# Optimization experiments

Hardware: AMD Instinct MI355X
Metric: run time of the kernel (lower is better)

## Reference

```python
import jax, jax.numpy as jnp
import numpy as np

N_NODES = 50000
N_EDGES = 500000
IN_DIM = 128
H1, C1 = 4, 64   # layer1: heads=4, out=64, concat -> 256
H2, C2 = 1, 64   # layer2: heads=1, out=64


def setup_inputs() -> dict:
    key = jax.random.key(0)
    ks = jax.random.split(key, 16)
    p = lambda k, shp: (jax.random.normal(k, shp, dtype=jnp.float32) * 0.1)
    return {
        "x": jax.random.normal(ks[0], (N_NODES, IN_DIM), dtype=jnp.float32),
        "edge_index": jax.random.randint(ks[1], (2, N_EDGES), 0, N_NODES, dtype=jnp.int32),
        "edge_attr": jax.random.uniform(ks[2], (N_EDGES, 1), dtype=jnp.float32),
        # layer 1 params
        "W1": p(ks[3], (IN_DIM, H1 * C1)),
        "We1": p(ks[4], (1, H1 * C1)),
        "as1": p(ks[5], (H1, C1)),
        "ad1": p(ks[6], (H1, C1)),
        "ae1": p(ks[7], (H1, C1)),
        "b1": jnp.zeros((H1 * C1,), dtype=jnp.float32),
        # layer 2 params
        "W2": p(ks[8], (H1 * C1, H2 * C2)),
        "We2": p(ks[9], (1, H2 * C2)),
        "as2": p(ks[10], (H2, C2)),
        "ad2": p(ks[11], (H2, C2)),
        "ae2": p(ks[12], (H2, C2)),
        "b2": jnp.zeros((H2 * C2,), dtype=jnp.float32),
    }


def _add_self_loops(src, dst, edge_attr, n):
    # PyG fill_value='mean': loop edge_attr = mean of incoming edge attrs per node
    cnt = jax.ops.segment_sum(jnp.ones((src.shape[0],), edge_attr.dtype), dst, num_segments=n)
    loop_attr = jax.ops.segment_sum(edge_attr, dst, num_segments=n) / jnp.maximum(cnt, 1.0)[:, None]
    idx = jnp.arange(n, dtype=src.dtype)
    return (jnp.concatenate([src, idx]), jnp.concatenate([dst, idx]),
            jnp.concatenate([edge_attr, loop_attr], axis=0))


def _gat_conv(x, src, dst, edge_attr, W, We, a_src, a_dst, a_edge, bias, heads, out_ch):
    n = x.shape[0]
    h = (x @ W).reshape(n, heads, out_ch)                      # [N,H,C]
    e = (edge_attr @ We).reshape(-1, heads, out_ch)            # [E,H,C]
    alpha = ((h * a_src).sum(-1)[src]                          # gather src score
             + (h * a_dst).sum(-1)[dst]                        # gather dst score
             + (e * a_edge).sum(-1))                           # [E,H]
    alpha = jax.nn.leaky_relu(alpha, 0.2)
    m = jax.ops.segment_max(alpha, dst, num_segments=n)        # per-target max
    alpha = jnp.exp(alpha - m[dst])
    denom = jax.ops.segment_sum(alpha, dst, num_segments=n)
    alpha = alpha / (denom[dst] + 1e-16)
    out = jax.ops.segment_sum(h[src] * alpha[..., None], dst, num_segments=n)
    return out.reshape(n, heads * out_ch) + bias


def reference(x, edge_index, edge_attr, W1, We1, as1, ad1, ae1, b1,
              W2, We2, as2, ad2, ae2, b2):
    src, dst = edge_index[0], edge_index[1]
    src, dst, ea = _add_self_loops(src, dst, edge_attr, x.shape[0])
    h = jax.nn.elu(_gat_conv(x, src, dst, ea, W1, We1, as1, ad1, ae1, b1, H1, C1))
    return _gat_conv(h, src, dst, ea, W2, We2, as2, ad2, ae2, b2, H2, C2)
```

## Files before the change

### kernel.cpp

```cpp
#include <hip/hip_runtime.h>
#include <math.h>

#define NN 50000
#define NE 500000
#define DIM 128
#define HC1 256
#define HC2 64
#define BCAP 64

typedef __attribute__((ext_vector_type(8))) short short8;
typedef __attribute__((ext_vector_type(4))) float floatx4;


__device__ __forceinline__ unsigned short f2bf(float f) {
  unsigned int u = __float_as_uint(f);
  unsigned int r = (u + 0x7FFFu + ((u >> 16) & 1u)) >> 16;
  return (unsigned short)r;
}
__device__ __forceinline__ float bf2f(unsigned short s) {
  return __uint_as_float(((unsigned int)s) << 16);
}


__global__ void k_bucket(const int* __restrict__ src, const int* __restrict__ dst,
                         const float* __restrict__ ea,
                         unsigned long long* __restrict__ P,
                         int2* __restrict__ ebuf) {
  int e = blockIdx.x * blockDim.x + threadIdx.x;
  if (e < NE) {
    int d = dst[e];
    float eav = ea[e];
    unsigned long long fx = (unsigned long long)(unsigned int)__float2uint_rn(eav * 16777216.0f);
    unsigned long long old = atomicAdd(&P[d], (1ULL << 40) | fx);
    int pos = (int)(old >> 40);
    if (pos < BCAP)
      ebuf[d * BCAP + pos] = make_int2(src[e], __float_as_int(eav));
  }
}

__device__ __forceinline__ void decodeP(unsigned long long p, int& cn, float& lea) {
  int c = (int)(p >> 40);
  cn = (c < BCAP) ? c : BCAP;
  float asum = (float)(p & 0xFFFFFFFFFFULL) * (1.0f / 16777216.0f);
  lea = asum / fmaxf((float)c, 1.0f);
}


__device__ __forceinline__ float waveReduce(float v) {
  v += __shfl_down(v, 32);
  v += __shfl_down(v, 16);
  v += __shfl_down(v, 8);
  v += __shfl_down(v, 4);
  v += __shfl_down(v, 2);
  v += __shfl_down(v, 1);
  return v;
}


__global__ __launch_bounds__(256) void k_prep(const float* __restrict__ W1,
                                              const float* __restrict__ W2,
                                              const float* __restrict__ We1,
                                              const float* __restrict__ ae1,
                                              const float* __restrict__ We2,
                                              const float* __restrict__ ae2,
                                              unsigned short* __restrict__ W1T,
                                              unsigned short* __restrict__ W2T,
                                              float* __restrict__ ce) {
  int b = blockIdx.x, t = threadIdx.x;
  if (b < 128) {
    int idx = b * 256 + t;
    int n = idx >> 7, k = idx & 127;
    W1T[idx] = f2bf(W1[k * 256 + n]);
  } else if (b < 192) {
    int idx = (b - 128) * 256 + t;
    int n = idx >> 8, k = idx & 255;
    W2T[idx] = f2bf(W2[k * 64 + n]);
  } else {
    int h = t >> 6, lane = t & 63;
    float p = We1[h * 64 + lane] * ae1[h * 64 + lane];
    p = waveReduce(p);
    if (lane == 0) ce[h] = p;
    if (h == 0) {
      float q = We2[lane] * ae2[lane];
      q = waveReduce(q);
      if (lane == 0) ce[4] = q;
    }
  }
}


__global__ __launch_bounds__(256) void k_gemm1m(const float* __restrict__ x,
                                                const unsigned short* __restrict__ W1T,
                                                const float* __restrict__ as1,
                                                const float* __restrict__ ad1,
                                                unsigned short* __restrict__ h1b,
                                                float* __restrict__ ss1,
                                                float* __restrict__ sd1) {
  __shared__ unsigned short As[64 * 136];
  int t = threadIdx.x;
  int wave = t >> 6, lane = t & 63;
  int q = lane >> 4, ln = lane & 15;
  int m0 = blockIdx.x * 64;
  int n0 = wave * 64;

  short8 bfr[4][4];
#pragma unroll
  for (int c = 0; c < 4; c++)
#pragma unroll
    for (int ks = 0; ks < 4; ks++)
      bfr[c][ks] = *(const short8*)&W1T[(n0 + c * 16 + ln) * 128 + ks * 32 + q * 8];

#pragma unroll
  for (int rep = 0; rep < 8; rep++) {
    int chunk = t + 256 * rep;
    int m = chunk >> 5, kk = (chunk & 31) * 4;
    int gr = m0 + m;
    float4 v = (gr < NN) ? *(const float4*)&x[gr * DIM + kk]
                         : make_float4(0.f, 0.f, 0.f, 0.f);
    ushort4 o;
    o.x = f2bf(v.x); o.y = f2bf(v.y); o.z = f2bf(v.z); o.w = f2bf(v.w);
    *(ushort4*)&As[m * 136 + kk] = o;
  }
  __syncthreads();

  floatx4 acc[4][4];
#pragma unroll
  for (int r = 0; r < 4; r++)
#pragma unroll
    for (int c = 0; c < 4; c++) acc[r][c] = (floatx4){0.f, 0.f, 0.f, 0.f};

#pragma unroll
  for (int ks = 0; ks < 4; ks++) {
    short8 afr[4];
#pragma unroll
    for (int r = 0; r < 4; r++)
      afr[r] = *(const short8*)&As[(r * 16 + ln) * 136 + ks * 32 + q * 8];
#pragma unroll
    for (int r = 0; r < 4; r++)
#pragma unroll
      for (int c = 0; c < 4; c++)
        acc[r][c] = __builtin_amdgcn_mfma_f32_16x16x32_bf16(afr[r], bfr[c][ks], acc[r][c], 0, 0, 0);
  }

  float as1v[4], ad1v[4];
#pragma unroll
  for (int c = 0; c < 4; c++) {
    as1v[c] = as1[n0 + c * 16 + ln];
    ad1v[c] = ad1[n0 + c * 16 + ln];
  }

#pragma unroll
  for (int r = 0; r < 4; r++) {
#pragma unroll
    for (int i = 0; i < 4; i++) {
      int gm = m0 + r * 16 + q * 4 + i;
      if (gm < NN) {
#pragma unroll
        for (int c = 0; c < 4; c++)
          h1b[gm * HC1 + n0 + c * 16 + ln] = f2bf(acc[r][c][i]);
      }
      float ps = acc[r][0][i] * as1v[0];
      float pd = acc[r][0][i] * ad1v[0];
#pragma unroll
      for (int c = 1; c < 4; c++) {
        ps = fmaf(acc[r][c][i], as1v[c], ps);
        pd = fmaf(acc[r][c][i], ad1v[c], pd);
      }
#pragma unroll
      for (int m = 1; m < 16; m <<= 1) {
        ps += __shfl_xor(ps, m);
        pd += __shfl_xor(pd, m);
      }
      if (ln == 0 && gm < NN) {
        ss1[gm * 4 + wave] = ps;
        sd1[gm * 4 + wave] = pd;
      }
    }
  }
}

__global__ __launch_bounds__(256) void k_gemm2m(const unsigned short* __restrict__ out1b,
                                                const unsigned short* __restrict__ W2T,
                                                const float* __restrict__ as2,
                                                const float* __restrict__ ad2,
                                                unsigned short* __restrict__ h2b,
                                                float* __restrict__ ss2,
                                                float* __restrict__ sd2) {
  __shared__ unsigned short As[64 * 264];
  __shared__ float ssp[4][64], sdp[4][64];
  int t = threadIdx.x;
  int wave = t >> 6, lane = t & 63;
  int q = lane >> 4, ln = lane & 15;
  int m0 = blockIdx.x * 64;
  int n0 = wave * 16;

  short8 bfr[8];
#pragma unroll
  for (int ks = 0; ks < 8; ks++)
    bfr[ks] = *(const short8*)&W2T[(n0 + ln) * 256 + ks * 32 + q * 8];

  short8 zero8 = {0, 0, 0, 0, 0, 0, 0, 0};
#pragma unroll
  for (int rep = 0; rep < 8; rep++) {
    int chunk = t + 256 * rep;
    int m = chunk >> 5, kk = (chunk & 31) * 8;
    int gr = m0 + m;
    short8 vv = (gr < NN) ? *(const short8*)&out1b[gr * 256 + kk] : zero8;
    *(short8*)&As[m * 264 + kk] = vv;
  }
  __syncthreads();

  floatx4 acc[4];
#pragma unroll
  for (int r = 0; r < 4; r++) acc[r] = (floatx4){0.f, 0.f, 0.f, 0.f};

#pragma unroll
  for (int ks = 0; ks < 8; ks++) {
#pragma unroll
    for (int r = 0; r < 4; r++) {
      short8 afr = *(const short8*)&As[(r * 16 + ln) * 264 + ks * 32 + q * 8];
      acc[r] = __builtin_amdgcn_mfma_f32_16x16x32_bf16(afr, bfr[ks], acc[r], 0, 0, 0);
    }
  }

  float as2v = as2[n0 + ln], ad2v = ad2[n0 + ln];
#pragma unroll
  for (int r = 0; r < 4; r++) {
#pragma unroll
    for (int i = 0; i < 4; i++) {
      int gm = m0 + r * 16 + q * 4 + i;
      if (gm < NN) h2b[gm * HC2 + n0 + ln] = f2bf(acc[r][i]);
      float ps = acc[r][i] * as2v;
      float pd = acc[r][i] * ad2v;
#pragma unroll
      for (int m = 1; m < 16; m <<= 1) {
        ps += __shfl_xor(ps, m);
        pd += __shfl_xor(pd, m);
      }
      if (ln == 0) {
        ssp[wave][r * 16 + q * 4 + i] = ps;
        sdp[wave][r * 16 + q * 4 + i] = pd;
      }
    }
  }
  __syncthreads();
  if (t < 64) {
    int gm = m0 + t;
    if (gm < NN) {
      ss2[gm] = ssp[0][t] + ssp[1][t] + ssp[2][t] + ssp[3][t];
      sd2[gm] = sdp[0][t] + sdp[1][t] + sdp[2][t] + sdp[3][t];
    }
  }
}


__global__ __launch_bounds__(256) void k_agg1(const unsigned short* __restrict__ h1b,
                                              const unsigned long long* __restrict__ P,
                                              const int2* __restrict__ ebuf,
                                              const float* __restrict__ ss1,
                                              const float* __restrict__ sd1,
                                              const float* __restrict__ ce,
                                              const float* __restrict__ b1,
                                              unsigned short* __restrict__ out1b) {
  int v = (blockIdx.x * blockDim.x + threadIdx.x) >> 6;
  int lane = threadIdx.x & 63;
  int h = lane >> 4;
  int c4 = lane * 4;
  int l16 = lane & 15;
  int vu = __builtin_amdgcn_readfirstlane(v);
  int cn; float lea;
  decodeP(P[vu], cn, lea);
  cn = __builtin_amdgcn_readfirstlane(cn);
  int beg = vu * BCAP;
  int end = beg + cn;
  float sdh = sd1[vu * 4 + h];
  float ceh = ce[h];
  float4 acc = make_float4(0.f, 0.f, 0.f, 0.f);
  float l = 0.f;

  for (int base = beg; base < end; base += 16) {
    int2 meta = ebuf[base + l16];
#pragma unroll
    for (int b4 = 0; b4 < 4; b4++) {
      if (base + b4 * 4 >= end) break;
      float ssv[4], ea4[4];
      ushort4 u[4];
      bool vld[4];
#pragma unroll
      for (int jj = 0; jj < 4; jj++) {
        int j = b4 * 4 + jj;
        bool val = (base + j < end);
        int sj = val ? __builtin_amdgcn_readlane(meta.x, j) : 0;
        ea4[jj] = __int_as_float(__builtin_amdgcn_readlane(meta.y, j));
        vld[jj] = val;
        ssv[jj] = ss1[sj * 4 + h];
        u[jj] = *(const ushort4*)&h1b[sj * HC1 + c4];
      }
#pragma unroll
      for (int jj = 0; jj < 4; jj++) {
        float x = fmaf(ea4[jj], ceh, ssv[jj] + sdh);
        x = fmaxf(x, 0.2f * x);
        float a = vld[jj] ? __expf(x) : 0.f;
        l += a;
        acc.x = fmaf(a, bf2f(u[jj].x), acc.x);
        acc.y = fmaf(a, bf2f(u[jj].y), acc.y);
        acc.z = fmaf(a, bf2f(u[jj].z), acc.z);
        acc.w = fmaf(a, bf2f(u[jj].w), acc.w);
      }
    }
  }
  {
    float x = fmaf(lea, ceh, ss1[vu * 4 + h] + sdh);
    x = fmaxf(x, 0.2f * x);
    float a = __expf(x);
    ushort4 u = *(const ushort4*)&h1b[vu * HC1 + c4];
    l += a;
    acc.x = fmaf(a, bf2f(u.x), acc.x);
    acc.y = fmaf(a, bf2f(u.y), acc.y);
    acc.z = fmaf(a, bf2f(u.z), acc.z);
    acc.w = fmaf(a, bf2f(u.w), acc.w);
  }
  float inv = 1.f / (l + 1e-16f);
  float4 bv = *(const float4*)&b1[c4];
  float4 o;
  o.x = acc.x * inv + bv.x;
  o.y = acc.y * inv + bv.y;
  o.z = acc.z * inv + bv.z;
  o.w = acc.w * inv + bv.w;
  o.x = (o.x > 0.f) ? o.x : expm1f(o.x);
  o.y = (o.y > 0.f) ? o.y : expm1f(o.y);
  o.z = (o.z > 0.f) ? o.z : expm1f(o.z);
  o.w = (o.w > 0.f) ? o.w : expm1f(o.w);
  ushort4 ob;
  ob.x = f2bf(o.x); ob.y = f2bf(o.y); ob.z = f2bf(o.z); ob.w = f2bf(o.w);
  *(ushort4*)&out1b[vu * HC1 + c4] = ob;
}

__global__ __launch_bounds__(256) void k_agg2(const unsigned short* __restrict__ h2b,
                                              const unsigned long long* __restrict__ P,
                                              const int2* __restrict__ ebuf,
                                              const float* __restrict__ ss2,
                                              const float* __restrict__ sd2,
                                              const float* __restrict__ ce,
                                              const float* __restrict__ b2,
                                              float* __restrict__ out) {
  int v = (blockIdx.x * blockDim.x + threadIdx.x) >> 6;
  int lane = threadIdx.x & 63;
  int g = lane >> 4;
  int c = lane & 15;
  int l16 = lane & 15;
  int vu = __builtin_amdgcn_readfirstlane(v);
  int cn; float lea;
  decodeP(P[vu], cn, lea);
  cn = __builtin_amdgcn_readfirstlane(cn);
  int beg = vu * BCAP;
  int end = beg + cn;
  float sdv = sd2[vu];
  float cev = ce[4];
  float4 acc = make_float4(0.f, 0.f, 0.f, 0.f);
  float l = 0.f;

  for (int base = beg; base < end; base += 16) {
    int nb = end - base;
    int2 meta = ebuf[base + l16];
    float ssv[4], eav[4];
    bool vld[4];
    ushort4 u[4];
#pragma unroll
    for (int sub = 0; sub < 4; sub++) {
      int j = sub * 4 + g;
      bool val = (j < nb);
      int sj = val ? __shfl(meta.x, j) : 0;
      eav[sub] = __int_as_float(__shfl(meta.y, j));
      vld[sub] = val;
      ssv[sub] = ss2[sj];
      u[sub] = *(const ushort4*)&h2b[sj * HC2 + c * 4];
    }
#pragma unroll
    for (int sub = 0; sub < 4; sub++) {
      float x = fmaf(eav[sub], cev, ssv[sub] + sdv);
      x = fmaxf(x, 0.2f * x);
      float a = vld[sub] ? __expf(x) : 0.f;
      l += a;
      acc.x = fmaf(a, bf2f(u[sub].x), acc.x);
      acc.y = fmaf(a, bf2f(u[sub].y), acc.y);
      acc.z = fmaf(a, bf2f(u[sub].z), acc.z);
      acc.w = fmaf(a, bf2f(u[sub].w), acc.w);
    }
  }
#pragma unroll
  for (int m = 16; m <= 32; m <<= 1) {
    acc.x += __shfl_xor(acc.x, m);
    acc.y += __shfl_xor(acc.y, m);
    acc.z += __shfl_xor(acc.z, m);
    acc.w += __shfl_xor(acc.w, m);
    l += __shfl_xor(l, m);
  }
  {
    float x = fmaf(lea, cev, ss2[vu] + sdv);
    x = fmaxf(x, 0.2f * x);
    float a = __expf(x);
    ushort4 us = *(const ushort4*)&h2b[vu * HC2 + c * 4];
    l += a;
    acc.x = fmaf(a, bf2f(us.x), acc.x);
    acc.y = fmaf(a, bf2f(us.y), acc.y);
    acc.z = fmaf(a, bf2f(us.z), acc.z);
    acc.w = fmaf(a, bf2f(us.w), acc.w);
  }
  if (g == 0) {
    float inv = 1.f / (l + 1e-16f);
    float4 bv = *(const float4*)&b2[c * 4];
    float4 o;
    o.x = acc.x * inv + bv.x;
    o.y = acc.y * inv + bv.y;
    o.z = acc.z * inv + bv.z;
    o.w = acc.w * inv + bv.w;
    *(float4*)&out[vu * HC2 + c * 4] = o;
  }
}


extern "C" void kernel_launch(void* const* d_in, const int* in_sizes, int n_in,
                              void* d_out, int out_size, void* d_ws, size_t ws_size,
                              hipStream_t stream) {
  const float* x   = (const float*)d_in[0];
  const int*   ei  = (const int*)d_in[1];
  const float* ea  = (const float*)d_in[2];
  const float* W1  = (const float*)d_in[3];
  const float* We1 = (const float*)d_in[4];
  const float* as1 = (const float*)d_in[5];
  const float* ad1 = (const float*)d_in[6];
  const float* ae1 = (const float*)d_in[7];
  const float* b1  = (const float*)d_in[8];
  const float* W2  = (const float*)d_in[9];
  const float* We2 = (const float*)d_in[10];
  const float* as2 = (const float*)d_in[11];
  const float* ad2 = (const float*)d_in[12];
  const float* ae2 = (const float*)d_in[13];
  const float* b2  = (const float*)d_in[14];
  const int* srcp = ei;
  const int* dstp = ei + NE;

  char* w = (char*)d_ws;
  unsigned long long* P = (unsigned long long*)(w + 0);
  float* ce      = (float*)(w + 400064);
  float* ss1     = (float*)(w + 400576);
  float* sd1     = (float*)(w + 1200576);
  float* ss2     = (float*)(w + 2000576);
  float* sd2     = (float*)(w + 2200576);
  int2*  ebuf    = (int2*) (w + 2400640);
  unsigned short* h1b   = (unsigned short*)(w + 28000640);
  unsigned short* out1b = (unsigned short*)(w + 53600640);
  unsigned short* h2b   = (unsigned short*)(w + 79200640);
  unsigned short* W1T   = (unsigned short*)(w + 85600640);
  unsigned short* W2T   = (unsigned short*)(w + 85666176);

  hipMemsetAsync(w, 0, 400000, stream);

  k_bucket<<<(NE + 255) / 256, 256, 0, stream>>>(srcp, dstp, ea, P, ebuf);
  k_prep<<<193, 256, 0, stream>>>(W1, W2, We1, ae1, We2, ae2, W1T, W2T, ce);

  k_gemm1m<<<(NN + 63) / 64, 256, 0, stream>>>(x, W1T, as1, ad1, h1b, ss1, sd1);
  k_agg1<<<(NN * 64 + 255) / 256, 256, 0, stream>>>(h1b, P, ebuf, ss1, sd1, ce, b1, out1b);

  k_gemm2m<<<(NN + 63) / 64, 256, 0, stream>>>(out1b, W2T, as2, ad2, h2b, ss2, sd2);
  k_agg2<<<(NN * 64 + 255) / 256, 256, 0, stream>>>(h2b, P, ebuf, ss2, sd2, ce, b2,
                                                    (float*)d_out);
}
```

Before: 232.7 us.

## Split layer-1 aggregation per head with head-major features and packed edge metadata

Stores layer-1 transformed features in a head-major layout and launches the first aggregation as one wave per (head, node), with blocks ordered head-first so each pass gathers from a smaller per-head feature slice. Packs each bucketed edge record into 32 bits (16-bit source index, 16-bit quantized edge attribute) to halve metadata traffic in both aggregations. Merges the edge bucketing kernel with the weight preparation kernel into one launch. The per-head split repeats metadata and score loads four times, and the quantized edge attribute adds small numerical error.

```diff
diff --git a/kernel.cpp b/kernel.cpp
--- a/kernel.cpp
+++ b/kernel.cpp
@@ -20,31 +20,6 @@
 __device__ __forceinline__ float bf2f(unsigned short s) {
   return __uint_as_float(((unsigned int)s) << 16);
 }
-
-
-__global__ void k_bucket(const int* __restrict__ src, const int* __restrict__ dst,
-                         const float* __restrict__ ea,
-                         unsigned long long* __restrict__ P,
-                         int2* __restrict__ ebuf) {
-  int e = blockIdx.x * blockDim.x + threadIdx.x;
-  if (e < NE) {
-    int d = dst[e];
-    float eav = ea[e];
-    unsigned long long fx = (unsigned long long)(unsigned int)__float2uint_rn(eav * 16777216.0f);
-    unsigned long long old = atomicAdd(&P[d], (1ULL << 40) | fx);
-    int pos = (int)(old >> 40);
-    if (pos < BCAP)
-      ebuf[d * BCAP + pos] = make_int2(src[e], __float_as_int(eav));
-  }
-}
-
-__device__ __forceinline__ void decodeP(unsigned long long p, int& cn, float& lea) {
-  int c = (int)(p >> 40);
-  cn = (c < BCAP) ? c : BCAP;
-  float asum = (float)(p & 0xFFFFFFFFFFULL) * (1.0f / 16777216.0f);
-  lea = asum / fmaxf((float)c, 1.0f);
-}
-
 
 __device__ __forceinline__ float waveReduce(float v) {
   v += __shfl_down(v, 32);
@@ -56,23 +31,50 @@
   return v;
 }
 
-
-__global__ __launch_bounds__(256) void k_prep(const float* __restrict__ W1,
-                                              const float* __restrict__ W2,
-                                              const float* __restrict__ We1,
-                                              const float* __restrict__ ae1,
-                                              const float* __restrict__ We2,
-                                              const float* __restrict__ ae2,
-                                              unsigned short* __restrict__ W1T,
-                                              unsigned short* __restrict__ W2T,
-                                              float* __restrict__ ce) {
+__device__ __forceinline__ void decodeP(unsigned long long p, int& cn, float& lea) {
+  int c = (int)(p >> 40);
+  cn = (c < BCAP) ? c : BCAP;
+  float asum = (float)(p & 0xFFFFFFFFFFULL) * (1.0f / 16777216.0f);
+  lea = asum / fmaxf((float)c, 1.0f);
+}
+
+
+#define NBUCKET ((NE + 255) / 256)
+
+__global__ __launch_bounds__(256) void k_build(const int* __restrict__ src,
+                                               const int* __restrict__ dst,
+                                               const float* __restrict__ ea,
+                                               unsigned long long* __restrict__ P,
+                                               unsigned int* __restrict__ ebuf,
+                                               const float* __restrict__ W1,
+                                               const float* __restrict__ W2,
+                                               const float* __restrict__ We1,
+                                               const float* __restrict__ ae1,
+                                               const float* __restrict__ We2,
+                                               const float* __restrict__ ae2,
+                                               unsigned short* __restrict__ W1T,
+                                               unsigned short* __restrict__ W2T,
+                                               float* __restrict__ ce) {
   int b = blockIdx.x, t = threadIdx.x;
-  if (b < 128) {
-    int idx = b * 256 + t;
+  if (b < NBUCKET) {
+    int e = b * 256 + t;
+    if (e < NE) {
+      int d = dst[e];
+      float eav = ea[e];
+      unsigned long long fx = (unsigned long long)(unsigned int)__float2uint_rn(eav * 16777216.0f);
+      unsigned long long old = atomicAdd(&P[d], (1ULL << 40) | fx);
+      int pos = (int)(old >> 40);
+      unsigned int ea16 = __float2uint_rn(eav * 65536.0f);
+      if (ea16 > 65535u) ea16 = 65535u;
+      if (pos < BCAP)
+        ebuf[d * BCAP + pos] = (ea16 << 16) | (unsigned int)src[e];
+    }
+  } else if (b < NBUCKET + 128) {
+    int idx = (b - NBUCKET) * 256 + t;
     int n = idx >> 7, k = idx & 127;
     W1T[idx] = f2bf(W1[k * 256 + n]);
-  } else if (b < 192) {
-    int idx = (b - 128) * 256 + t;
+  } else if (b < NBUCKET + 192) {
+    int idx = (b - NBUCKET - 128) * 256 + t;
     int n = idx >> 8, k = idx & 255;
     W2T[idx] = f2bf(W2[k * 64 + n]);
   } else {
@@ -93,7 +95,7 @@
                                                 const unsigned short* __restrict__ W1T,
                                                 const float* __restrict__ as1,
                                                 const float* __restrict__ ad1,
-                                                unsigned short* __restrict__ h1b,
+                                                unsigned short* __restrict__ h1h,
                                                 float* __restrict__ ss1,
                                                 float* __restrict__ sd1) {
   __shared__ unsigned short As[64 * 136];
@@ -157,7 +159,7 @@
       if (gm < NN) {
 #pragma unroll
         for (int c = 0; c < 4; c++)
-          h1b[gm * HC1 + n0 + c * 16 + ln] = f2bf(acc[r][c][i]);
+          h1h[(wave * NN + gm) * 64 + c * 16 + ln] = f2bf(acc[r][c][i]);
       }
       float ps = acc[r][0][i] * as1v[0];
       float pd = acc[r][0][i] * ad1v[0];
@@ -254,47 +256,45 @@
 }
 
 
-__global__ __launch_bounds__(256) void k_agg1(const unsigned short* __restrict__ h1b,
+__global__ __launch_bounds__(256) void k_agg1(const unsigned short* __restrict__ h1h,
                                               const unsigned long long* __restrict__ P,
-                                              const int2* __restrict__ ebuf,
+                                              const unsigned int* __restrict__ ebuf,
                                               const float* __restrict__ ss1,
                                               const float* __restrict__ sd1,
                                               const float* __restrict__ ce,
                                               const float* __restrict__ b1,
                                               unsigned short* __restrict__ out1b) {
-  int v = (blockIdx.x * blockDim.x + threadIdx.x) >> 6;
-  int lane = threadIdx.x & 63;
-  int h = lane >> 4;
-  int c4 = lane * 4;
+  int wave = threadIdx.x >> 6, lane = threadIdx.x & 63;
+  int head = blockIdx.x / 12500;
+  int vu = (blockIdx.x % 12500) * 4 + wave;
   int l16 = lane & 15;
-  int vu = __builtin_amdgcn_readfirstlane(v);
   int cn; float lea;
   decodeP(P[vu], cn, lea);
   cn = __builtin_amdgcn_readfirstlane(cn);
   int beg = vu * BCAP;
   int end = beg + cn;
-  float sdh = sd1[vu * 4 + h];
-  float ceh = ce[h];
-  float4 acc = make_float4(0.f, 0.f, 0.f, 0.f);
-  float l = 0.f;
+  float sdh = sd1[vu * 4 + head];
+  float ceh = ce[head];
+  const unsigned short* hs = h1h + (size_t)head * NN * 64;
+  float acc = 0.f, l = 0.f;
 
   for (int base = beg; base < end; base += 16) {
-    int2 meta = ebuf[base + l16];
+    unsigned int meta = ebuf[base + l16];
 #pragma unroll
     for (int b4 = 0; b4 < 4; b4++) {
       if (base + b4 * 4 >= end) break;
-      float ssv[4], ea4[4];
-      ushort4 u[4];
+      float ssv[4], ea4[4], hv[4];
       bool vld[4];
 #pragma unroll
       for (int jj = 0; jj < 4; jj++) {
         int j = b4 * 4 + jj;
         bool val = (base + j < end);
-        int sj = val ? __builtin_amdgcn_readlane(meta.x, j) : 0;
-        ea4[jj] = __int_as_float(__builtin_amdgcn_readlane(meta.y, j));
+        unsigned int m = __builtin_amdgcn_readlane(meta, j);
+        int sj = val ? (int)(m & 0xFFFFu) : 0;
+        ea4[jj] = (float)(m >> 16) * (1.0f / 65536.0f);
         vld[jj] = val;
-        ssv[jj] = ss1[sj * 4 + h];
-        u[jj] = *(const ushort4*)&h1b[sj * HC1 + c4];
+        ssv[jj] = ss1[sj * 4 + head];
+        hv[jj] = bf2f(hs[sj * 64 + lane]);
       }
 #pragma unroll
       for (int jj = 0; jj < 4; jj++) {
@@ -302,43 +302,26 @@
         x = fmaxf(x, 0.2f * x);
         float a = vld[jj] ? __expf(x) : 0.f;
         l += a;
-        acc.x = fmaf(a, bf2f(u[jj].x), acc.x);
-        acc.y = fmaf(a, bf2f(u[jj].y), acc.y);
-        acc.z = fmaf(a, bf2f(u[jj].z), acc.z);
-        acc.w = fmaf(a, bf2f(u[jj].w), acc.w);
+        acc = fmaf(a, hv[jj], acc);
       }
     }
   }
   {
-    float x = fmaf(lea, ceh, ss1[vu * 4 + h] + sdh);
+    float x = fmaf(lea, ceh, ss1[vu * 4 + head] + sdh);
     x = fmaxf(x, 0.2f * x);
     float a = __expf(x);
-    ushort4 u = *(const ushort4*)&h1b[vu * HC1 + c4];
+    float hv = bf2f(hs[vu * 64 + lane]);
     l += a;
-    acc.x = fmaf(a, bf2f(u.x), acc.x);
-    acc.y = fmaf(a, bf2f(u.y), acc.y);
-    acc.z = fmaf(a, bf2f(u.z), acc.z);
-    acc.w = fmaf(a, bf2f(u.w), acc.w);
-  }
-  float inv = 1.f / (l + 1e-16f);
-  float4 bv = *(const float4*)&b1[c4];
-  float4 o;
-  o.x = acc.x * inv + bv.x;
-  o.y = acc.y * inv + bv.y;
-  o.z = acc.z * inv + bv.z;
-  o.w = acc.w * inv + bv.w;
-  o.x = (o.x > 0.f) ? o.x : expm1f(o.x);
-  o.y = (o.y > 0.f) ? o.y : expm1f(o.y);
-  o.z = (o.z > 0.f) ? o.z : expm1f(o.z);
-  o.w = (o.w > 0.f) ? o.w : expm1f(o.w);
-  ushort4 ob;
-  ob.x = f2bf(o.x); ob.y = f2bf(o.y); ob.z = f2bf(o.z); ob.w = f2bf(o.w);
-  *(ushort4*)&out1b[vu * HC1 + c4] = ob;
+    acc = fmaf(a, hv, acc);
+  }
+  float o = acc / (l + 1e-16f) + b1[head * 64 + lane];
+  o = (o > 0.f) ? o : expm1f(o);
+  out1b[vu * HC1 + head * 64 + lane] = f2bf(o);
 }
 
 __global__ __launch_bounds__(256) void k_agg2(const unsigned short* __restrict__ h2b,
                                               const unsigned long long* __restrict__ P,
-                                              const int2* __restrict__ ebuf,
+                                              const unsigned int* __restrict__ ebuf,
                                               const float* __restrict__ ss2,
                                               const float* __restrict__ sd2,
                                               const float* __restrict__ ce,
@@ -362,7 +345,7 @@
 
   for (int base = beg; base < end; base += 16) {
     int nb = end - base;
-    int2 meta = ebuf[base + l16];
+    unsigned int meta = ebuf[base + l16];
     float ssv[4], eav[4];
     bool vld[4];
     ushort4 u[4];
@@ -370,8 +353,9 @@
     for (int sub = 0; sub < 4; sub++) {
       int j = sub * 4 + g;
       bool val = (j < nb);
-      int sj = val ? __shfl(meta.x, j) : 0;
-      eav[sub] = __int_as_float(__shfl(meta.y, j));
+      unsigned int m = (unsigned int)__shfl((int)meta, j);
+      int sj = val ? (int)(m & 0xFFFFu) : 0;
+      eav[sub] = (float)(m >> 16) * (1.0f / 65536.0f);
       vld[sub] = val;
       ssv[sub] = ss2[sj];
       u[sub] = *(const ushort4*)&h2b[sj * HC2 + c * 4];
@@ -448,20 +432,21 @@
   float* sd1     = (float*)(w + 1200576);
   float* ss2     = (float*)(w + 2000576);
   float* sd2     = (float*)(w + 2200576);
-  int2*  ebuf    = (int2*) (w + 2400640);
-  unsigned short* h1b   = (unsigned short*)(w + 28000640);
-  unsigned short* out1b = (unsigned short*)(w + 53600640);
-  unsigned short* h2b   = (unsigned short*)(w + 79200640);
-  unsigned short* W1T   = (unsigned short*)(w + 85600640);
-  unsigned short* W2T   = (unsigned short*)(w + 85666176);
+  unsigned int* ebuf = (unsigned int*)(w + 2400640);
+  unsigned short* h1h   = (unsigned short*)(w + 15200640);
+  unsigned short* out1b = (unsigned short*)(w + 40800640);
+  unsigned short* h2b   = (unsigned short*)(w + 66400640);
+  unsigned short* W1T   = (unsigned short*)(w + 72800640);
+  unsigned short* W2T   = (unsigned short*)(w + 72866176);
 
   hipMemsetAsync(w, 0, 400000, stream);
 
-  k_bucket<<<(NE + 255) / 256, 256, 0, stream>>>(srcp, dstp, ea, P, ebuf);
-  k_prep<<<193, 256, 0, stream>>>(W1, W2, We1, ae1, We2, ae2, W1T, W2T, ce);
-
-  k_gemm1m<<<(NN + 63) / 64, 256, 0, stream>>>(x, W1T, as1, ad1, h1b, ss1, sd1);
-  k_agg1<<<(NN * 64 + 255) / 256, 256, 0, stream>>>(h1b, P, ebuf, ss1, sd1, ce, b1, out1b);
+  k_build<<<NBUCKET + 193, 256, 0, stream>>>(srcp, dstp, ea, P, ebuf,
+                                             W1, W2, We1, ae1, We2, ae2,
+                                             W1T, W2T, ce);
+
+  k_gemm1m<<<(NN + 63) / 64, 256, 0, stream>>>(x, W1T, as1, ad1, h1h, ss1, sd1);
+  k_agg1<<<12500 * 4, 256, 0, stream>>>(h1h, P, ebuf, ss1, sd1, ce, b1, out1b);
 
   k_gemm2m<<<(NN + 63) / 64, 256, 0, stream>>>(out1b, W2T, as2, ad2, h2b, ss2, sd2);
   k_agg2<<<(NN * 64 + 255) / 256, 256, 0, stream>>>(h2b, P, ebuf, ss2, sd2, ce, b2,
```

Measured after the change: 280.3 us. +20.5%, slower.
